# Optimization experiments

Measured on AMD Instinct MI355X. Metric: run time of the kernel, lower is better.

Reference implementation:

```python
import jax, jax.numpy as jnp
import numpy as np

B, S, D, H, V = 4, 1024, 1024, 16, 1024
HD = D // H  # head_dim = 64
FF = 4 * D


def _layer_norm(x, g, b, eps=1e-5):
    mu = jnp.mean(x, axis=-1, keepdims=True)
    var = jnp.var(x, axis=-1, keepdims=True)
    return (x - mu) * jax.lax.rsqrt(var + eps) * g + b


def _pos_encoding(seq_len, d_model):
    # sinusoidal PE, matching PositionalEncoding buffer construction
    pos = jnp.arange(seq_len, dtype=jnp.float32)[:, None]
    div = jnp.exp(jnp.arange(0, d_model, 2, dtype=jnp.float32) * (-np.log(10000.0) / d_model))
    pe = jnp.zeros((seq_len, d_model), dtype=jnp.float32)
    pe = pe.at[:, 0::2].set(jnp.sin(pos * div))
    pe = pe.at[:, 1::2].set(jnp.cos(pos * div))
    return pe


def setup_inputs() -> dict:
    key = jax.random.key(0)
    ks = jax.random.split(key, 12)
    sc = 0.02
    return {
        "inputs": jax.random.randint(ks[0], (B, S), 0, V, dtype=jnp.int32),
        "targets": jax.random.randint(ks[1], (B, S), 0, V, dtype=jnp.int32),
        "wte": jax.random.normal(ks[2], (V, D), jnp.float32) * sc,
        "wq": jax.random.normal(ks[3], (D, D), jnp.float32) * sc,
        "bq": jnp.zeros((D,), jnp.float32),
        "wk": jax.random.normal(ks[4], (D, D), jnp.float32) * sc,
        "bk": jnp.zeros((D,), jnp.float32),
        "wv": jax.random.normal(ks[5], (D, D), jnp.float32) * sc,
        "bv": jnp.zeros((D,), jnp.float32),
        "wo": jax.random.normal(ks[6], (D, D), jnp.float32) * sc,
        "bo": jnp.zeros((D,), jnp.float32),
        "w1": jax.random.normal(ks[7], (D, FF), jnp.float32) * sc,
        "b1": jnp.zeros((FF,), jnp.float32),
        "w2": jax.random.normal(ks[8], (FF, D), jnp.float32) * sc,
        "b2": jnp.zeros((D,), jnp.float32),
        "ln1_g": jnp.ones((D,), jnp.float32),
        "ln1_b": jnp.zeros((D,), jnp.float32),
        "ln2_g": jnp.ones((D,), jnp.float32),
        "ln2_b": jnp.zeros((D,), jnp.float32),
    }


def reference(inputs, targets, wte, wq, bq, wk, bk, wv, bv, wo, bo,
              w1, b1, w2, b2, ln1_g, ln1_b, ln2_g, ln2_b):
    # embedding + positional encoding
    x = wte[inputs] + _pos_encoding(S, D)  # [B,S,D]

    # naive causal multi-head attention (dropout = identity in eval)
    q = (x @ wq + bq).reshape(B, S, H, HD)
    k = (x @ wk + bk).reshape(B, S, H, HD)
    v = (x @ wv + bv).reshape(B, S, H, HD)
    scores = jnp.einsum('bqhd,bkhd->bhqk', q, k) / np.sqrt(HD)  # [B,H,S,S]
    causal = jnp.tril(jnp.ones((S, S), dtype=bool))
    scores = jnp.where(causal, scores, -jnp.inf)
    attn = jax.nn.softmax(scores, axis=-1)
    ctx = jnp.einsum('bhqk,bkhd->bqhd', attn, v).reshape(B, S, D)
    att_out = ctx @ wo + bo

    # residual + LN1, FFN + GELU, residual + LN2
    adn = _layer_norm(x + att_out, ln1_g, ln1_b)
    h = jax.nn.gelu(adn @ w1 + b1, approximate=False) @ w2 + b2
    logits = _layer_norm(h + adn, ln2_g, ln2_b)

    # cross-entropy over d_model(=vocab) classes
    logits_flat = logits.reshape(B * S, D)
    tgt = targets.reshape(B * S)
    logp = jax.nn.log_softmax(logits_flat, axis=-1)
    loss = -jnp.mean(jnp.take_along_axis(logp, tgt[:, None], axis=-1))
    return logits_flat, loss
```

## Files before the change

### kernel.cpp

```cpp
#include <hip/hip_runtime.h>
#include <math.h>

#define BB 4
#define SS 1024
#define DD 1024
#define HH 16
#define HDIM 64
#define FF 4096
#define MM 4096

typedef short bf16x8 __attribute__((ext_vector_type(8)));
typedef short bf16x4 __attribute__((ext_vector_type(4)));
typedef float f32x4  __attribute__((ext_vector_type(4)));

static __device__ __forceinline__ short f2bf(float f){
  unsigned u = __float_as_uint(f);
  u += 0x7FFFu + ((u >> 16) & 1u);
  return (short)(u >> 16);
}
static __device__ __forceinline__ float b2f(short s){
  return __uint_as_float(((unsigned)(unsigned short)s) << 16);
}

static __device__ __forceinline__ float erf_fast(float x){
  float ax = fabsf(x);
  float t  = __builtin_amdgcn_rcpf(1.0f + 0.3275911f * ax);
  float p  = t * (0.254829592f + t * (-0.284496736f + t * (1.421413741f +
             t * (-1.453152027f + t * 1.061405429f))));
  float e  = 1.0f - p * __expf(-ax * ax);
  return copysignf(e, x);
}

static __device__ __forceinline__ void gl_lds16(const short* g, short* l){
  __builtin_amdgcn_global_load_lds((const __attribute__((address_space(1))) unsigned int*)g,
                                   (__attribute__((address_space(3))) unsigned int*)l,
                                   16, 0, 0);
}

#define MFMA_BF16 __builtin_amdgcn_mfma_f32_16x16x32_bf16

__global__ __launch_bounds__(256) void trans_all_kernel(
    const float* __restrict__ wq, const float* __restrict__ wk,
    const float* __restrict__ wv, const float* __restrict__ wo,
    const float* __restrict__ w1, const float* __restrict__ w2,
    short* __restrict__ wqkvt, short* __restrict__ wot,
    short* __restrict__ w1t,   short* __restrict__ w2t){
  __shared__ float t[32][33];
  int idx = blockIdx.x;
  const float* src; short* dst; int R, C, cx, ry;
  if (idx < 4096){
    int wsel = idx >> 10, tt = idx & 1023;
    cx = tt & 31; ry = tt >> 5; R = 1024; C = 1024;
    src = (wsel == 0) ? wq : (wsel == 1) ? wk : (wsel == 2) ? wv : wo;
    dst = (wsel == 3) ? wot : wqkvt + (size_t)wsel * 1024 * 1024;
  } else if (idx < 8192){
    int tt = idx - 4096; cx = tt & 127; ry = tt >> 7; R = 1024; C = 4096;
    src = w1; dst = w1t;
  } else {
    int tt = idx - 8192; cx = tt & 31; ry = tt >> 5; R = 4096; C = 1024;
    src = w2; dst = w2t;
  }
  int c0 = cx * 32, r0 = ry * 32;
  int tx = threadIdx.x, ty = threadIdx.y;
#pragma unroll
  for (int i = 0; i < 32; i += 8)
    t[ty + i][tx] = src[(size_t)(r0 + ty + i) * C + (c0 + tx)];
  __syncthreads();
#pragma unroll
  for (int i = 0; i < 32; i += 8)
    dst[(size_t)(c0 + ty + i) * R + (r0 + tx)] = f2bf(t[tx][ty + i]);
}

__global__ __launch_bounds__(256) void concat_bias_kernel(const float* __restrict__ a,
                                                          const float* __restrict__ b,
                                                          const float* __restrict__ c,
                                                          float* __restrict__ dst){
  int t = blockIdx.x * 256 + threadIdx.x;
  float v = (t < 1024) ? a[t] : (t < 2048 ? b[t - 1024] : c[t - 2048]);
  dst[t] = v;
}

__global__ __launch_bounds__(256) void embed_kernel(const int* __restrict__ inputs,
                                                    const float* __restrict__ wte,
                                                    short* __restrict__ xb){
  int idx4 = blockIdx.x * 256 + threadIdx.x;
  int row = idx4 >> 8;
  int d   = (idx4 & 255) * 4;
  int s   = row & (SS - 1);
  int tok = inputs[row];
  float4 w = *(const float4*)&wte[(size_t)tok * DD + d];
  const float cdiv = -9.210340371976184f / 512.0f;
  int i0 = d >> 1;
  float ang0 = (float)s * expf((float)i0 * cdiv);
  float ang1 = (float)s * expf((float)(i0 + 1) * cdiv);
  float x0 = w.x + sinf(ang0);
  float x1 = w.y + cosf(ang0);
  float x2 = w.z + sinf(ang1);
  float x3 = w.w + cosf(ang1);
  bf16x4 sb; sb[0]=f2bf(x0); sb[1]=f2bf(x1); sb[2]=f2bf(x2); sb[3]=f2bf(x3);
  *(bf16x4*)&xb[(size_t)row * DD + d] = sb;
}

template<int MODE, bool GELU, bool ADDBIAS>
__global__ __launch_bounds__(512, 2) void gemm256_kernel(const short* __restrict__ A,
    const short* __restrict__ Bt, const float* __restrict__ bias,
    short* __restrict__ o0, short* __restrict__ o1,
    short* __restrict__ o2, short* __restrict__ o3,
    short* __restrict__ qo, short* __restrict__ ko, short* __restrict__ vto,
    int M, int N, int K, int Kc){
  __shared__ __align__(16) short lds[8 * 8192];
  int tid = threadIdx.x;
  int lid = blockIdx.y * gridDim.x + blockIdx.x;
  int cpx = (gridDim.x * gridDim.y) >> 3;
  int swz = (lid & 7) * cpx + (lid >> 3);
  int n0 = (swz % gridDim.x) * 256;
  int m0 = (swz / gridDim.x) * 256;
  int bz = blockIdx.z;
  int kbeg = bz * Kc;
  int w = tid >> 6, lane = tid & 63, lr = lane & 15, lg = lane >> 4;
  int wm = w >> 2, wn = w & 3;
  f32x4 acc[8][4] = {};

  int sr = lane >> 3;
  int sg = (lane & 7) ^ sr;
  auto STAGE_HALF = [&](int buf, int typ, int half, int kt){
    const short* s0 = (typ ? Bt : A) + (size_t)kbeg + sg * 8;
    int rb = (typ ? n0 : m0) + half * 128 + w * 8 + sr;
#pragma unroll
    for (int j = 0; j < 2; j++)
      gl_lds16(s0 + (size_t)(rb + j * 64) * K + kt * 64,
               &lds[(((buf << 2) | (typ << 1) | half) << 13) + (j << 12) + (w << 9)]);
  };

  int nt = Kc >> 6;
  STAGE_HALF(0, 0, 0, 0); STAGE_HALF(0, 0, 1, 0);
  STAGE_HALF(0, 1, 0, 0); STAGE_HALF(0, 1, 1, 0);
  STAGE_HALF(1, 0, 0, 1); STAGE_HALF(1, 0, 1, 1);
  STAGE_HALF(1, 1, 0, 1); STAGE_HALF(1, 1, 1, 1);
  asm volatile("s_waitcnt vmcnt(8)" ::: "memory");
  __builtin_amdgcn_s_barrier();

  int lr64 = lr * 64;
  int ck0 = ((lg     ) ^ (lr & 7)) * 8;
  int ck1 = ((lg + 4 ) ^ (lr & 7)) * 8;
  int brow = (wn & 1) << 12;

  bf16x8 Alo[4][2], Ahi[4][2], Blo[2][2], Bhi[2][2];

#define ABASE(b) ((((b) << 2) | wm) << 13) + lr64
#define BBASE(b) ((((b) << 2) | 2 | (wn >> 1)) << 13) + brow + lr64
#define RD_ALO(b) { int ab_ = ABASE(b); _Pragma("unroll") for (int fi_ = 0; fi_ < 4; fi_++){ \
    Alo[fi_][0] = *(const bf16x8*)&lds[ab_ + fi_ * 1024 + ck0]; \
    Alo[fi_][1] = *(const bf16x8*)&lds[ab_ + fi_ * 1024 + ck1]; } }
#define RD_AHI(b) { int ab_ = ABASE(b); _Pragma("unroll") for (int fi_ = 0; fi_ < 4; fi_++){ \
    Ahi[fi_][0] = *(const bf16x8*)&lds[ab_ + (fi_ + 4) * 1024 + ck0]; \
    Ahi[fi_][1] = *(const bf16x8*)&lds[ab_ + (fi_ + 4) * 1024 + ck1]; } }
#define RD_BLO(b) { int bb_ = BBASE(b); _Pragma("unroll") for (int ni_ = 0; ni_ < 2; ni_++){ \
    Blo[ni_][0] = *(const bf16x8*)&lds[bb_ + ni_ * 1024 + ck0]; \
    Blo[ni_][1] = *(const bf16x8*)&lds[bb_ + ni_ * 1024 + ck1]; } }
#define RD_BHI(b) { int bb_ = BBASE(b); _Pragma("unroll") for (int ni_ = 0; ni_ < 2; ni_++){ \
    Bhi[ni_][0] = *(const bf16x8*)&lds[bb_ + (ni_ + 2) * 1024 + ck0]; \
    Bhi[ni_][1] = *(const bf16x8*)&lds[bb_ + (ni_ + 2) * 1024 + ck1]; } }
#define QUAD(MB, NB, AF, BF) \
    __builtin_amdgcn_s_setprio(1); \
    _Pragma("unroll") for (int mi_ = 0; mi_ < 4; mi_++) \
      _Pragma("unroll") for (int ni_ = 0; ni_ < 2; ni_++){ \
        acc[mi_ + MB][ni_ + NB] = MFMA_BF16(AF[mi_][0], BF[ni_][0], acc[mi_ + MB][ni_ + NB], 0, 0, 0); \
        acc[mi_ + MB][ni_ + NB] = MFMA_BF16(AF[mi_][1], BF[ni_][1], acc[mi_ + MB][ni_ + NB], 0, 0, 0); } \
    __builtin_amdgcn_s_setprio(0);

  RD_ALO(0); RD_BLO(0);

  for (int t = 0; t < nt; t++){
    int b = t & 1, bn = b ^ 1;
    RD_AHI(b);
    asm volatile("s_waitcnt lgkmcnt(8)" ::: "memory");
    __builtin_amdgcn_sched_barrier(0);
    QUAD(0, 0, Alo, Blo);
    __builtin_amdgcn_s_barrier();
    RD_BHI(b);
    if (t + 2 < nt){ STAGE_HALF(b, 0, 0, t + 2); STAGE_HALF(b, 0, 1, t + 2); }
    asm volatile("s_waitcnt lgkmcnt(4)" ::: "memory");
    __builtin_amdgcn_sched_barrier(0);
    QUAD(4, 0, Ahi, Blo);
    __builtin_amdgcn_s_barrier();
    if (t + 2 < nt) asm volatile("s_waitcnt vmcnt(4)" ::: "memory");
    else            asm volatile("s_waitcnt vmcnt(0)" ::: "memory");
    if (t + 2 < nt){ STAGE_HALF(b, 1, 0, t + 2); STAGE_HALF(b, 1, 1, t + 2); }
    asm volatile("s_waitcnt lgkmcnt(0)" ::: "memory");
    __builtin_amdgcn_sched_barrier(0);
    QUAD(4, 2, Ahi, Bhi);
    __builtin_amdgcn_s_barrier();
    QUAD(0, 2, Alo, Bhi);
    __builtin_amdgcn_sched_barrier(0);
    if (t + 1 < nt){ RD_ALO(bn); RD_BLO(bn); }
    __builtin_amdgcn_s_barrier();
  }
#undef QUAD
#undef RD_BHI
#undef RD_BLO
#undef RD_AHI
#undef RD_ALO
#undef BBASE
#undef ABASE

  short* slab = (MODE == 1) ? ((bz == 0) ? o0 : (bz == 1) ? o1 : (bz == 2) ? o2 : o3) : o0;
  bool addb = ADDBIAS && (MODE != 1 || bz == 0);
#pragma unroll
  for (int mi = 0; mi < 8; mi++){
#pragma unroll
    for (int ni = 0; ni < 4; ni++){
      int ng = n0 + wn * 64 + ni * 16 + lr;
      float bv = addb ? bias[ng] : 0.0f;
      int mg0 = m0 + wm * 128 + mi * 16 + 4 * lg;
      if (MODE == 2){
        int sel = n0 >> 10;
        if (sel == 2){
          int d = ng & 1023; int hh = d >> 6, nn = d & 63;
          int bI = mg0 >> 10, sI = mg0 & 1023;
          bf16x4 pk;
#pragma unroll
          for (int r = 0; r < 4; r++) pk[r] = f2bf(acc[mi][ni][r] + bv);
          *(bf16x4*)&vto[(((size_t)(bI * HH + hh)) * HDIM + nn) * SS + sI] = pk;
        } else {
          short* dst = (sel == 0) ? qo : ko;
#pragma unroll
          for (int r = 0; r < 4; r++)
            dst[(size_t)(mg0 + r) * DD + (ng & 1023)] = f2bf(acc[mi][ni][r] + bv);
        }
      } else {
#pragma unroll
        for (int r = 0; r < 4; r++){
          float v = acc[mi][ni][r] + bv;
          if (GELU) v = 0.5f * v * (1.0f + erf_fast(v * 0.70710678118654752f));
          slab[(size_t)(mg0 + r) * N + ng] = f2bf(v);
        }
      }
    }
  }
}

__global__ __launch_bounds__(256) void attn_kernel(const short* __restrict__ qb,
                                                   const short* __restrict__ kb,
                                                   const short* __restrict__ vtb,
                                                   short* __restrict__ ctxb){
  __shared__ __align__(16) short k_lds[2][64 * 64];
  __shared__ __align__(16) short v_lds[2][64 * 64];
  __shared__ __align__(16) short p_lds[4][2][16 * 72];
  int qp = blockIdx.x, h = blockIdx.y, b = blockIdx.z;
  int Tlo = qp, Thi = 15 - qp;
  int tid = threadIdx.x, w = tid >> 6, lane = tid & 63, lr = lane & 15, lg = lane >> 4;

  const short* kp0 = kb  + (size_t)b * SS * DD + h * HDIM;
  const short* vt0 = vtb + (size_t)(b * HH + h) * HDIM * SS;

  bf16x8 qf0[2], qf1[2];
#pragma unroll
  for (int ti = 0; ti < 2; ti++){
    int T = ti ? Thi : Tlo;
    const short* qp_ = qb + ((size_t)(b * SS + T * 64 + w * 16 + lr) * DD + h * HDIM);
    qf0[ti] = *(const bf16x8*)&qp_[lg * 8];
    qf1[ti] = *(const bf16x8*)&qp_[32 + lg * 8];
  }

  float m[2][4], l[2][4];
  f32x4 acc[2][4] = {};
#pragma unroll
  for (int ti = 0; ti < 2; ti++)
#pragma unroll
    for (int r = 0; r < 4; r++){ m[ti][r] = -1e30f; l[ti][r] = 0.0f; }

  int srow8 = lane >> 3;
  int sjs   = (lane & 7) ^ srow8;
  auto STAGE = [&](int buf, int kt){
#pragma unroll
    for (int i = 0; i < 2; i++){
      int rb  = (w + 4 * i) * 8;
      int row = rb + srow8;
      gl_lds16(kp0 + (size_t)(kt * 64 + row) * DD + sjs * 8, &k_lds[buf][rb * 64]);
      gl_lds16(vt0 + (size_t)row * SS + kt * 64 + sjs * 8,   &v_lds[buf][rb * 64]);
    }
  };

  int cur = 0;
  STAGE(0, 0);
  asm volatile("s_waitcnt vmcnt(0)" ::: "memory");
  __syncthreads();

  bf16x8 pf0[2], pf1[2];
  for (int kt = 0; kt <= Thi; kt++){
    if (kt < Thi) STAGE(cur ^ 1, kt + 1);

    bf16x8 kf0[4], kf1[4];
#pragma unroll
    for (int sub = 0; sub < 4; sub++){
      int r = sub * 16 + lr;
      kf0[sub] = *(const bf16x8*)&k_lds[cur][r * 64 + ((lg     ^ (r & 7)) * 8)];
      kf1[sub] = *(const bf16x8*)&k_lds[cur][r * 64 + (((lg+4) ^ (r & 7)) * 8)];
    }

#pragma unroll
    for (int ti = 0; ti < 2; ti++){
      int T = ti ? Thi : Tlo;
      if (kt > T) continue;
      f32x4 sc4[4];
#pragma unroll
      for (int sub = 0; sub < 4; sub++){
        f32x4 t = {};
        t = MFMA_BF16(qf0[ti], kf0[sub], t, 0, 0, 0);
        t = MFMA_BF16(qf1[ti], kf1[sub], t, 0, 0, 0);
#pragma unroll
        for (int r = 0; r < 4; r++) t[r] *= 0.125f;
        sc4[sub] = t;
      }
      if (kt == T){
#pragma unroll
        for (int sub = 0; sub < 4; sub++)
#pragma unroll
          for (int r = 0; r < 4; r++)
            if (16 * sub + lr > 16 * w + 4 * lg + r) sc4[sub][r] = -1e30f;
      }

      float pm[4];
#pragma unroll
      for (int r = 0; r < 4; r++)
        pm[r] = fmaxf(fmaxf(sc4[0][r], sc4[1][r]), fmaxf(sc4[2][r], sc4[3][r]));
#pragma unroll
      for (int off = 1; off < 16; off <<= 1)
#pragma unroll
        for (int r = 0; r < 4; r++) pm[r] = fmaxf(pm[r], __shfl_xor(pm[r], off));

      float scl[4], rs[4];
#pragma unroll
      for (int r = 0; r < 4; r++){
        float mn = fmaxf(m[ti][r], pm[r]);
        scl[r] = __expf(m[ti][r] - mn);
        m[ti][r] = mn;
        rs[r] = 0.0f;
      }
#pragma unroll
      for (int sub = 0; sub < 4; sub++)
#pragma unroll
        for (int r = 0; r < 4; r++){
          float p = __expf(sc4[sub][r] - m[ti][r]);
          sc4[sub][r] = p;
          rs[r] += p;
        }
#pragma unroll
      for (int off = 1; off < 16; off <<= 1)
#pragma unroll
        for (int r = 0; r < 4; r++) rs[r] += __shfl_xor(rs[r], off);
#pragma unroll
      for (int r = 0; r < 4; r++) l[ti][r] = l[ti][r] * scl[r] + rs[r];
#pragma unroll
      for (int nb = 0; nb < 4; nb++)
#pragma unroll
        for (int r = 0; r < 4; r++) acc[ti][nb][r] *= scl[r];

      short* pw = &p_lds[w][ti][0];
#pragma unroll
      for (int sub = 0; sub < 4; sub++)
#pragma unroll
        for (int r = 0; r < 4; r++)
          pw[(4 * lg + r) * 72 + sub * 16 + lr] = f2bf(sc4[sub][r]);
      pf0[ti] = *(const bf16x8*)&pw[lr * 72 + lg * 8];
      pf1[ti] = *(const bf16x8*)&pw[lr * 72 + 32 + lg * 8];
    }

    bf16x8 vf0[4], vf1[4];
#pragma unroll
    for (int nb = 0; nb < 4; nb++){
      int r = nb * 16 + lr;
      vf0[nb] = *(const bf16x8*)&v_lds[cur][r * 64 + ((lg     ^ (r & 7)) * 8)];
      vf1[nb] = *(const bf16x8*)&v_lds[cur][r * 64 + (((lg+4) ^ (r & 7)) * 8)];
    }

#pragma unroll
    for (int ti = 0; ti < 2; ti++){
      int T = ti ? Thi : Tlo;
      if (kt > T) continue;
#pragma unroll
      for (int nb = 0; nb < 4; nb++){
        acc[ti][nb] = MFMA_BF16(pf0[ti], vf0[nb], acc[ti][nb], 0, 0, 0);
        acc[ti][nb] = MFMA_BF16(pf1[ti], vf1[nb], acc[ti][nb], 0, 0, 0);
      }
    }

    asm volatile("s_waitcnt vmcnt(0)" ::: "memory");
    __syncthreads();
    cur ^= 1;
  }

#pragma unroll
  for (int ti = 0; ti < 2; ti++){
    int T = ti ? Thi : Tlo;
#pragma unroll
    for (int r = 0; r < 4; r++){
      float inv = 1.0f / l[ti][r];
      int row = T * 64 + w * 16 + 4 * lg + r;
#pragma unroll
      for (int nb = 0; nb < 4; nb++)
        ctxb[(size_t)(b * SS + row) * DD + h * HDIM + nb * 16 + lr] = f2bf(acc[ti][nb][r] * inv);
    }
  }
}

template<int NPART, bool WF32, bool LOSS>
__global__ __launch_bounds__(256) void ln_kernel(const short* __restrict__ p0,
                                                 const short* __restrict__ p1,
                                                 const short* __restrict__ p2,
                                                 const short* __restrict__ p3,
                                                 const short* __restrict__ resb,
                                                 const float* __restrict__ g,
                                                 const float* __restrict__ be,
                                                 float* __restrict__ of,
                                                 short* __restrict__ ob,
                                                 const int* __restrict__ tgt,
                                                 float* __restrict__ lrow){
  int row = blockIdx.x, tid = threadIdx.x;
  size_t base = (size_t)row * DD + tid * 4;
  bf16x4 rv = *(const bf16x4*)&resb[base];
  float x0 = b2f(rv[0]), x1 = b2f(rv[1]), x2 = b2f(rv[2]), x3 = b2f(rv[3]);
  const short* ps[4] = {p0, p1, p2, p3};
#pragma unroll
  for (int p = 0; p < NPART; p++){
    bf16x4 pv = *(const bf16x4*)&ps[p][base];
    x0 += b2f(pv[0]); x1 += b2f(pv[1]); x2 += b2f(pv[2]); x3 += b2f(pv[3]);
  }
  float s = x0 + x1 + x2 + x3;
  float q = x0 * x0 + x1 * x1 + x2 * x2 + x3 * x3;
#pragma unroll
  for (int off = 32; off; off >>= 1){ s += __shfl_xor(s, off); q += __shfl_xor(q, off); }
  __shared__ float red[9];
  if ((tid & 63) == 0){ red[tid >> 6] = s; red[4 + (tid >> 6)] = q; }
  __syncthreads();
  s = red[0] + red[1] + red[2] + red[3];
  q = red[4] + red[5] + red[6] + red[7];
  float mean = s * (1.0f / DD);
  float var  = q * (1.0f / DD) - mean * mean;
  float rstd = rsqrtf(var + 1e-5f);
  float4 gv  = *(const float4*)&g[tid * 4];
  float4 bev = *(const float4*)&be[tid * 4];
  float y0 = (x0 - mean) * rstd * gv.x + bev.x;
  float y1 = (x1 - mean) * rstd * gv.y + bev.y;
  float y2 = (x2 - mean) * rstd * gv.z + bev.z;
  float y3 = (x3 - mean) * rstd * gv.w + bev.w;
  if (WF32){
    *(float4*)&of[base] = make_float4(y0, y1, y2, y3);
  } else {
    bf16x4 sb; sb[0]=f2bf(y0); sb[1]=f2bf(y1); sb[2]=f2bf(y2); sb[3]=f2bf(y3);
    *(bf16x4*)&ob[base] = sb;
  }
  if (LOSS){
    __syncthreads();
    float mx = fmaxf(fmaxf(y0, y1), fmaxf(y2, y3));
#pragma unroll
    for (int off = 32; off; off >>= 1) mx = fmaxf(mx, __shfl_xor(mx, off));
    if ((tid & 63) == 0) red[tid >> 6] = mx;
    int t = tgt[row];
    if (tid == (t >> 2))
      red[8] = ((t & 3) == 0) ? y0 : ((t & 3) == 1) ? y1 : ((t & 3) == 2) ? y2 : y3;
    __syncthreads();
    mx = fmaxf(fmaxf(red[0], red[1]), fmaxf(red[2], red[3]));
    float se = __expf(y0 - mx) + __expf(y1 - mx) + __expf(y2 - mx) + __expf(y3 - mx);
#pragma unroll
    for (int off = 32; off; off >>= 1) se += __shfl_xor(se, off);
    if ((tid & 63) == 0) red[4 + (tid >> 6)] = se;
    __syncthreads();
    if (tid == 0){
      float tot = red[4] + red[5] + red[6] + red[7];
      lrow[row] = mx + logf(tot) - red[8];
    }
  }
}

__global__ __launch_bounds__(256) void loss_reduce_kernel(const float* __restrict__ pr,
                                                          float* __restrict__ outp){
  int tid = threadIdx.x;
  float s = 0.0f;
  for (int i = tid; i < MM; i += 256) s += pr[i];
#pragma unroll
  for (int off = 32; off; off >>= 1) s += __shfl_xor(s, off);
  __shared__ float red[4];
  if ((tid & 63) == 0) red[tid >> 6] = s;
  __syncthreads();
  if (tid == 0) outp[0] = (red[0] + red[1] + red[2] + red[3]) * (1.0f / MM);
}

extern "C" void kernel_launch(void* const* d_in, const int* in_sizes, int n_in,
                              void* d_out, int out_size, void* d_ws, size_t ws_size,
                              hipStream_t stream){
  const int*   inputs  = (const int*)  d_in[0];
  const int*   targets = (const int*)  d_in[1];
  const float* wte     = (const float*)d_in[2];
  const float* wq      = (const float*)d_in[3];
  const float* bq      = (const float*)d_in[4];
  const float* wk      = (const float*)d_in[5];
  const float* bk      = (const float*)d_in[6];
  const float* wv      = (const float*)d_in[7];
  const float* bvv     = (const float*)d_in[8];
  const float* wo      = (const float*)d_in[9];
  const float* bo      = (const float*)d_in[10];
  const float* w1      = (const float*)d_in[11];
  const float* b1      = (const float*)d_in[12];
  const float* w2      = (const float*)d_in[13];
  const float* b2      = (const float*)d_in[14];
  const float* ln1g    = (const float*)d_in[15];
  const float* ln1b    = (const float*)d_in[16];
  const float* ln2g    = (const float*)d_in[17];
  const float* ln2b    = (const float*)d_in[18];
  float* out = (float*)d_out;

  char* ws = (char*)d_ws;
  const size_t MB = 1024 * 1024;
  short* wqkvt = (short*)(ws + 0 * MB);
  short* wot   = (short*)(ws + 6 * MB);
  short* w1t   = (short*)(ws + 8 * MB);
  short* w2t   = (short*)(ws + 16 * MB);
  short* xb    = (short*)(ws + 24 * MB);
  short* qbuf  = (short*)(ws + 32 * MB);
  short* kbuf  = (short*)(ws + 40 * MB);
  short* vtb   = (short*)(ws + 48 * MB);
  short* ctxb  = (short*)(ws + 56 * MB);
  short* pr0   = (short*)(ws + 64 * MB);
  short* pr1   = (short*)(ws + 72 * MB);
  short* pr2   = (short*)(ws + 80 * MB);
  short* pr3   = (short*)(ws + 88 * MB);
  short* adnb  = (short*)(ws + 96 * MB);
  short* h1b   = (short*)(ws + 32 * MB);
  short* hs0   = (short*)(ws + 64 * MB);
  short* hs1   = (short*)(ws + 72 * MB);
  short* hs2   = (short*)(ws + 80 * MB);
  short* hs3   = (short*)(ws + 88 * MB);
  float* lrow  = (float*)(ws + 104 * MB);
  float* bqkv  = (float*)(ws + 105 * MB);

  trans_all_kernel<<<12288, dim3(32, 8), 0, stream>>>(
      wq, wk, wv, wo, w1, w2, wqkvt, wot, w1t, w2t);
  concat_bias_kernel<<<12, 256, 0, stream>>>(bq, bk, bvv, bqkv);

  embed_kernel<<<4096, 256, 0, stream>>>(inputs, wte, xb);

  gemm256_kernel<2, false, true><<<dim3(12, 16), 512, 0, stream>>>(
      xb, wqkvt, bqkv, nullptr, nullptr, nullptr, nullptr,
      qbuf, kbuf, vtb, MM, 3 * DD, DD, DD);

  attn_kernel<<<dim3(8, 16, 4), 256, 0, stream>>>(qbuf, kbuf, vtb, ctxb);

  gemm256_kernel<1, false, true><<<dim3(4, 16, 4), 512, 0, stream>>>(
      ctxb, wot, bo, pr0, pr1, pr2, pr3,
      nullptr, nullptr, nullptr, MM, DD, DD, 256);

  ln_kernel<4, false, false><<<4096, 256, 0, stream>>>(
      pr0, pr1, pr2, pr3, xb, ln1g, ln1b, nullptr, adnb, nullptr, nullptr);

  gemm256_kernel<0, true, true><<<dim3(16, 16), 512, 0, stream>>>(
      adnb, w1t, b1, h1b, nullptr, nullptr, nullptr,
      nullptr, nullptr, nullptr, MM, FF, DD, DD);

  gemm256_kernel<1, false, true><<<dim3(4, 16, 4), 512, 0, stream>>>(
      h1b, w2t, b2, hs0, hs1, hs2, hs3,
      nullptr, nullptr, nullptr, MM, DD, FF, 1024);

  ln_kernel<4, true, true><<<4096, 256, 0, stream>>>(
      hs0, hs1, hs2, hs3, adnb, ln2g, ln2b, out, nullptr, targets, lrow);

  loss_reduce_kernel<<<1, 256, 0, stream>>>(lrow, out + (size_t)MM * DD);
}
```

Measured before the change: 225.7 us.

## Restructure causal attention: one query tile per block, lazy rescale, MFMA row sums

Folds the 1/sqrt(head_dim) scale into Q in the QKV GEMM epilogue, and launches one 64-row query tile per block (16 blocks per head) instead of pairing a low and a high tile for load balance. The online softmax now skips rescaling the accumulator unless the running max grows by more than 8, and computes row sums with an MFMA against a ones vector instead of shuffle reductions. It also raises wave priority around the MFMA sections. The exchange is causal load imbalance across blocks and bf16-rounded probabilities being summed for the normaliser.

```diff
diff --git a/kernel.cpp b/kernel.cpp
--- a/kernel.cpp
+++ b/kernel.cpp
@@ -224,9 +224,10 @@
           *(bf16x4*)&vto[(((size_t)(bI * HH + hh)) * HDIM + nn) * SS + sI] = pk;
         } else {
           short* dst = (sel == 0) ? qo : ko;
+          float qscl = (sel == 0) ? 0.125f : 1.0f;
 #pragma unroll
           for (int r = 0; r < 4; r++)
-            dst[(size_t)(mg0 + r) * DD + (ng & 1023)] = f2bf(acc[mi][ni][r] + bv);
+            dst[(size_t)(mg0 + r) * DD + (ng & 1023)] = f2bf((acc[mi][ni][r] + bv) * qscl);
         }
       } else {
 #pragma unroll
@@ -246,29 +247,25 @@
                                                    short* __restrict__ ctxb){
   __shared__ __align__(16) short k_lds[2][64 * 64];
   __shared__ __align__(16) short v_lds[2][64 * 64];
-  __shared__ __align__(16) short p_lds[4][2][16 * 72];
-  int qp = blockIdx.x, h = blockIdx.y, b = blockIdx.z;
-  int Tlo = qp, Thi = 15 - qp;
+  __shared__ __align__(16) short p_lds[4][16 * 72];
+  int qt = blockIdx.x, h = blockIdx.y, b = blockIdx.z;
   int tid = threadIdx.x, w = tid >> 6, lane = tid & 63, lr = lane & 15, lg = lane >> 4;
 
   const short* kp0 = kb  + (size_t)b * SS * DD + h * HDIM;
   const short* vt0 = vtb + (size_t)(b * HH + h) * HDIM * SS;
 
-  bf16x8 qf0[2], qf1[2];
-#pragma unroll
-  for (int ti = 0; ti < 2; ti++){
-    int T = ti ? Thi : Tlo;
-    const short* qp_ = qb + ((size_t)(b * SS + T * 64 + w * 16 + lr) * DD + h * HDIM);
-    qf0[ti] = *(const bf16x8*)&qp_[lg * 8];
-    qf1[ti] = *(const bf16x8*)&qp_[32 + lg * 8];
-  }
-
-  float m[2][4], l[2][4];
-  f32x4 acc[2][4] = {};
-#pragma unroll
-  for (int ti = 0; ti < 2; ti++)
-#pragma unroll
-    for (int r = 0; r < 4; r++){ m[ti][r] = -1e30f; l[ti][r] = 0.0f; }
+  const short* qp_ = qb + ((size_t)(b * SS + qt * 64 + w * 16 + lr) * DD + h * HDIM);
+  bf16x8 qf0 = *(const bf16x8*)&qp_[lg * 8];
+  bf16x8 qf1 = *(const bf16x8*)&qp_[32 + lg * 8];
+
+  bf16x8 ones;
+#pragma unroll
+  for (int j = 0; j < 8; j++) ones[j] = (short)0x3F80;
+
+  float m[4], l[4];
+  f32x4 acc[4] = {};
+#pragma unroll
+  for (int r = 0; r < 4; r++){ m[r] = -1e30f; l[r] = 0.0f; }
 
   int srow8 = lane >> 3;
   int sjs   = (lane & 7) ^ srow8;
@@ -287,9 +284,9 @@
   asm volatile("s_waitcnt vmcnt(0)" ::: "memory");
   __syncthreads();
 
-  bf16x8 pf0[2], pf1[2];
-  for (int kt = 0; kt <= Thi; kt++){
-    if (kt < Thi) STAGE(cur ^ 1, kt + 1);
+  short* pw = &p_lds[w][0];
+  for (int kt = 0; kt <= qt; kt++){
+    if (kt < qt) STAGE(cur ^ 1, kt + 1);
 
     bf16x8 kf0[4], kf1[4];
 #pragma unroll
@@ -299,73 +296,59 @@
       kf1[sub] = *(const bf16x8*)&k_lds[cur][r * 64 + (((lg+4) ^ (r & 7)) * 8)];
     }
 
-#pragma unroll
-    for (int ti = 0; ti < 2; ti++){
-      int T = ti ? Thi : Tlo;
-      if (kt > T) continue;
-      f32x4 sc4[4];
-#pragma unroll
-      for (int sub = 0; sub < 4; sub++){
-        f32x4 t = {};
-        t = MFMA_BF16(qf0[ti], kf0[sub], t, 0, 0, 0);
-        t = MFMA_BF16(qf1[ti], kf1[sub], t, 0, 0, 0);
-#pragma unroll
-        for (int r = 0; r < 4; r++) t[r] *= 0.125f;
-        sc4[sub] = t;
+    f32x4 sc4[4];
+    __builtin_amdgcn_s_setprio(1);
+#pragma unroll
+    for (int sub = 0; sub < 4; sub++){
+      f32x4 t = {};
+      t = MFMA_BF16(qf0, kf0[sub], t, 0, 0, 0);
+      t = MFMA_BF16(qf1, kf1[sub], t, 0, 0, 0);
+      sc4[sub] = t;
+    }
+    __builtin_amdgcn_s_setprio(0);
+
+    if (kt == qt){
+#pragma unroll
+      for (int sub = 0; sub < 4; sub++)
+#pragma unroll
+        for (int r = 0; r < 4; r++)
+          if (16 * sub + lr > 16 * w + 4 * lg + r) sc4[sub][r] = -1e30f;
+    }
+
+    float pm[4];
+#pragma unroll
+    for (int r = 0; r < 4; r++)
+      pm[r] = fmaxf(fmaxf(sc4[0][r], sc4[1][r]), fmaxf(sc4[2][r], sc4[3][r]));
+#pragma unroll
+    for (int off = 1; off < 16; off <<= 1)
+#pragma unroll
+      for (int r = 0; r < 4; r++) pm[r] = fmaxf(pm[r], __shfl_xor(pm[r], off));
+
+    float dmax = fmaxf(fmaxf(pm[0] - m[0], pm[1] - m[1]),
+                       fmaxf(pm[2] - m[2], pm[3] - m[3]));
+    if (!__all(dmax <= 8.0f)){
+      float scl[4];
+#pragma unroll
+      for (int r = 0; r < 4; r++){
+        float mn = fmaxf(m[r], pm[r]);
+        scl[r] = __expf(m[r] - mn);
+        m[r] = mn;
+        l[r] *= scl[r];
       }
-      if (kt == T){
-#pragma unroll
-        for (int sub = 0; sub < 4; sub++)
-#pragma unroll
-          for (int r = 0; r < 4; r++)
-            if (16 * sub + lr > 16 * w + 4 * lg + r) sc4[sub][r] = -1e30f;
-      }
-
-      float pm[4];
+#pragma unroll
+      for (int nb = 0; nb < 4; nb++)
+#pragma unroll
+        for (int r = 0; r < 4; r++) acc[nb][r] *= scl[r];
+    }
+
+#pragma unroll
+    for (int sub = 0; sub < 4; sub++)
 #pragma unroll
       for (int r = 0; r < 4; r++)
-        pm[r] = fmaxf(fmaxf(sc4[0][r], sc4[1][r]), fmaxf(sc4[2][r], sc4[3][r]));
-#pragma unroll
-      for (int off = 1; off < 16; off <<= 1)
-#pragma unroll
-        for (int r = 0; r < 4; r++) pm[r] = fmaxf(pm[r], __shfl_xor(pm[r], off));
-
-      float scl[4], rs[4];
-#pragma unroll
-      for (int r = 0; r < 4; r++){
-        float mn = fmaxf(m[ti][r], pm[r]);
-        scl[r] = __expf(m[ti][r] - mn);
-        m[ti][r] = mn;
-        rs[r] = 0.0f;
-      }
-#pragma unroll
-      for (int sub = 0; sub < 4; sub++)
-#pragma unroll
-        for (int r = 0; r < 4; r++){
-          float p = __expf(sc4[sub][r] - m[ti][r]);
-          sc4[sub][r] = p;
-          rs[r] += p;
-        }
-#pragma unroll
-      for (int off = 1; off < 16; off <<= 1)
-#pragma unroll
-        for (int r = 0; r < 4; r++) rs[r] += __shfl_xor(rs[r], off);
-#pragma unroll
-      for (int r = 0; r < 4; r++) l[ti][r] = l[ti][r] * scl[r] + rs[r];
-#pragma unroll
-      for (int nb = 0; nb < 4; nb++)
-#pragma unroll
-        for (int r = 0; r < 4; r++) acc[ti][nb][r] *= scl[r];
-
-      short* pw = &p_lds[w][ti][0];
-#pragma unroll
-      for (int sub = 0; sub < 4; sub++)
-#pragma unroll
-        for (int r = 0; r < 4; r++)
-          pw[(4 * lg + r) * 72 + sub * 16 + lr] = f2bf(sc4[sub][r]);
-      pf0[ti] = *(const bf16x8*)&pw[lr * 72 + lg * 8];
-      pf1[ti] = *(const bf16x8*)&pw[lr * 72 + 32 + lg * 8];
-    }
+        pw[(4 * lg + r) * 72 + sub * 16 + lr] = f2bf(__expf(sc4[sub][r] - m[r]));
+
+    bf16x8 pf0 = *(const bf16x8*)&pw[lr * 72 + lg * 8];
+    bf16x8 pf1 = *(const bf16x8*)&pw[lr * 72 + 32 + lg * 8];
 
     bf16x8 vf0[4], vf1[4];
 #pragma unroll
@@ -375,16 +358,18 @@
       vf1[nb] = *(const bf16x8*)&v_lds[cur][r * 64 + (((lg+4) ^ (r & 7)) * 8)];
     }
 
-#pragma unroll
-    for (int ti = 0; ti < 2; ti++){
-      int T = ti ? Thi : Tlo;
-      if (kt > T) continue;
-#pragma unroll
-      for (int nb = 0; nb < 4; nb++){
-        acc[ti][nb] = MFMA_BF16(pf0[ti], vf0[nb], acc[ti][nb], 0, 0, 0);
-        acc[ti][nb] = MFMA_BF16(pf1[ti], vf1[nb], acc[ti][nb], 0, 0, 0);
-      }
-    }
+    f32x4 rsum = {};
+    __builtin_amdgcn_s_setprio(1);
+    rsum = MFMA_BF16(pf0, ones, rsum, 0, 0, 0);
+    rsum = MFMA_BF16(pf1, ones, rsum, 0, 0, 0);
+#pragma unroll
+    for (int nb = 0; nb < 4; nb++){
+      acc[nb] = MFMA_BF16(pf0, vf0[nb], acc[nb], 0, 0, 0);
+      acc[nb] = MFMA_BF16(pf1, vf1[nb], acc[nb], 0, 0, 0);
+    }
+    __builtin_amdgcn_s_setprio(0);
+#pragma unroll
+    for (int r = 0; r < 4; r++) l[r] += rsum[r];
 
     asm volatile("s_waitcnt vmcnt(0)" ::: "memory");
     __syncthreads();
@@ -392,16 +377,12 @@
   }
 
 #pragma unroll
-  for (int ti = 0; ti < 2; ti++){
-    int T = ti ? Thi : Tlo;
-#pragma unroll
-    for (int r = 0; r < 4; r++){
-      float inv = 1.0f / l[ti][r];
-      int row = T * 64 + w * 16 + 4 * lg + r;
-#pragma unroll
-      for (int nb = 0; nb < 4; nb++)
-        ctxb[(size_t)(b * SS + row) * DD + h * HDIM + nb * 16 + lr] = f2bf(acc[ti][nb][r] * inv);
-    }
+  for (int r = 0; r < 4; r++){
+    float inv = 1.0f / l[r];
+    int row = qt * 64 + w * 16 + 4 * lg + r;
+#pragma unroll
+    for (int nb = 0; nb < 4; nb++)
+      ctxb[(size_t)(b * SS + row) * DD + h * HDIM + nb * 16 + lr] = f2bf(acc[nb][r] * inv);
   }
 }
 
@@ -545,7 +526,7 @@
       xb, wqkvt, bqkv, nullptr, nullptr, nullptr, nullptr,
       qbuf, kbuf, vtb, MM, 3 * DD, DD, DD);
 
-  attn_kernel<<<dim3(8, 16, 4), 256, 0, stream>>>(qbuf, kbuf, vtb, ctxb);
+  attn_kernel<<<dim3(16, 16, 4), 256, 0, stream>>>(qbuf, kbuf, vtb, ctxb);
 
   gemm256_kernel<1, false, true><<<dim3(4, 16, 4), 512, 0, stream>>>(
       ctxb, wot, bo, pr0, pr1, pr2, pr3,
```

New measurement: 240.2 us. 6.4% more time.

## Fold softmax scale into Q, lazy rescale, MFMA row sums, setprio

Applied to the files above, without the earlier changes.

Folds the 1/sqrt(d) scale into the Q projection epilogue, computes softmax row sums with an MFMA against a ones vector instead of shuffle reductions, and skips rescaling the running max and accumulator unless some row's max grows by more than a threshold (lazy rescale). It also raises wave priority around MFMA blocks. This removes VALU and cross-lane shuffle work from the attention inner loop. The trade-off is that exp values can exceed 1 by up to e^8 before a rescale, which costs bf16 precision, and scaling Q before bf16 rounding slightly changes numerics.

```diff
diff --git a/kernel.cpp b/kernel.cpp
--- a/kernel.cpp
+++ b/kernel.cpp
@@ -224,9 +224,10 @@
           *(bf16x4*)&vto[(((size_t)(bI * HH + hh)) * HDIM + nn) * SS + sI] = pk;
         } else {
           short* dst = (sel == 0) ? qo : ko;
+          float qscl = (sel == 0) ? 0.125f : 1.0f;
 #pragma unroll
           for (int r = 0; r < 4; r++)
-            dst[(size_t)(mg0 + r) * DD + (ng & 1023)] = f2bf(acc[mi][ni][r] + bv);
+            dst[(size_t)(mg0 + r) * DD + (ng & 1023)] = f2bf((acc[mi][ni][r] + bv) * qscl);
         }
       } else {
 #pragma unroll
@@ -263,6 +264,10 @@
     qf1[ti] = *(const bf16x8*)&qp_[32 + lg * 8];
   }
 
+  bf16x8 ones;
+#pragma unroll
+  for (int j = 0; j < 8; j++) ones[j] = (short)0x3F80;
+
   float m[2][4], l[2][4];
   f32x4 acc[2][4] = {};
 #pragma unroll
@@ -304,15 +309,15 @@
       int T = ti ? Thi : Tlo;
       if (kt > T) continue;
       f32x4 sc4[4];
+      __builtin_amdgcn_s_setprio(1);
 #pragma unroll
       for (int sub = 0; sub < 4; sub++){
         f32x4 t = {};
         t = MFMA_BF16(qf0[ti], kf0[sub], t, 0, 0, 0);
         t = MFMA_BF16(qf1[ti], kf1[sub], t, 0, 0, 0);
-#pragma unroll
-        for (int r = 0; r < 4; r++) t[r] *= 0.125f;
         sc4[sub] = t;
       }
+      __builtin_amdgcn_s_setprio(0);
       if (kt == T){
 #pragma unroll
         for (int sub = 0; sub < 4; sub++)
@@ -330,39 +335,29 @@
 #pragma unroll
         for (int r = 0; r < 4; r++) pm[r] = fmaxf(pm[r], __shfl_xor(pm[r], off));
 
-      float scl[4], rs[4];
-#pragma unroll
-      for (int r = 0; r < 4; r++){
-        float mn = fmaxf(m[ti][r], pm[r]);
-        scl[r] = __expf(m[ti][r] - mn);
-        m[ti][r] = mn;
-        rs[r] = 0.0f;
+      float dmax = fmaxf(fmaxf(pm[0] - m[ti][0], pm[1] - m[ti][1]),
+                         fmaxf(pm[2] - m[ti][2], pm[3] - m[ti][3]));
+      if (!__all(dmax <= 8.0f)){
+        float scl[4];
+#pragma unroll
+        for (int r = 0; r < 4; r++){
+          float mn = fmaxf(m[ti][r], pm[r]);
+          scl[r] = __expf(m[ti][r] - mn);
+          m[ti][r] = mn;
+          l[ti][r] *= scl[r];
+        }
+#pragma unroll
+        for (int nb = 0; nb < 4; nb++)
+#pragma unroll
+          for (int r = 0; r < 4; r++) acc[ti][nb][r] *= scl[r];
       }
+
+      short* pw = &p_lds[w][ti][0];
 #pragma unroll
       for (int sub = 0; sub < 4; sub++)
 #pragma unroll
-        for (int r = 0; r < 4; r++){
-          float p = __expf(sc4[sub][r] - m[ti][r]);
-          sc4[sub][r] = p;
-          rs[r] += p;
-        }
-#pragma unroll
-      for (int off = 1; off < 16; off <<= 1)
-#pragma unroll
-        for (int r = 0; r < 4; r++) rs[r] += __shfl_xor(rs[r], off);
-#pragma unroll
-      for (int r = 0; r < 4; r++) l[ti][r] = l[ti][r] * scl[r] + rs[r];
-#pragma unroll
-      for (int nb = 0; nb < 4; nb++)
-#pragma unroll
-        for (int r = 0; r < 4; r++) acc[ti][nb][r] *= scl[r];
-
-      short* pw = &p_lds[w][ti][0];
-#pragma unroll
-      for (int sub = 0; sub < 4; sub++)
-#pragma unroll
         for (int r = 0; r < 4; r++)
-          pw[(4 * lg + r) * 72 + sub * 16 + lr] = f2bf(sc4[sub][r]);
+          pw[(4 * lg + r) * 72 + sub * 16 + lr] = f2bf(__expf(sc4[sub][r] - m[ti][r]));
       pf0[ti] = *(const bf16x8*)&pw[lr * 72 + lg * 8];
       pf1[ti] = *(const bf16x8*)&pw[lr * 72 + 32 + lg * 8];
     }
@@ -379,11 +374,18 @@
     for (int ti = 0; ti < 2; ti++){
       int T = ti ? Thi : Tlo;
       if (kt > T) continue;
+      f32x4 rsum = {};
+      __builtin_amdgcn_s_setprio(1);
+      rsum = MFMA_BF16(pf0[ti], ones, rsum, 0, 0, 0);
+      rsum = MFMA_BF16(pf1[ti], ones, rsum, 0, 0, 0);
 #pragma unroll
       for (int nb = 0; nb < 4; nb++){
         acc[ti][nb] = MFMA_BF16(pf0[ti], vf0[nb], acc[ti][nb], 0, 0, 0);
         acc[ti][nb] = MFMA_BF16(pf1[ti], vf1[nb], acc[ti][nb], 0, 0, 0);
       }
+      __builtin_amdgcn_s_setprio(0);
+#pragma unroll
+      for (int r = 0; r < 4; r++) l[ti][r] += rsum[r];
     }
 
     asm volatile("s_waitcnt vmcnt(0)" ::: "memory");
```

After: 219.2 us, median of 2. 1.03x faster.
